# Performance work log

Measured on AMD Instinct MI355X. Metric: run time of the kernel, lower is better.

## Reference

```python
import jax, jax.numpy as jnp
import numpy as np

D_MODEL = 512
D_STATE = 128
D_CONV = 4
EXPAND = 2
NL = 10
HEADDIM = 64
D_INNER = EXPAND * D_MODEL            # 1024
NHEADS = D_INNER // HEADDIM           # 16
CONV_DIM = D_INNER + 2 * D_STATE      # 1280
D_PROJ = 2 * D_INNER + 2 * D_STATE + NHEADS  # 2320
BATCH = 8
IN_S, TOK_S = 3647, 64                # -> 57 tokens
IN_G, TOK_G = 18, 2                   # -> 9 tokens
NCLS = 55
CA_HEADS = 8
EPS = 1e-5


def setup_inputs() -> dict:
    key = jax.random.key(0)
    ks = iter(jax.random.split(key, 80))
    nrm = lambda shape, s=0.02: jax.random.normal(next(ks), shape, jnp.float32) * s
    inp = {
        "x_spectra": jax.random.normal(next(ks), (BATCH, IN_S), jnp.float32),
        "x_gaia": jax.random.normal(next(ks), (BATCH, IN_G), jnp.float32),
        "tok_w_s": nrm((TOK_S, D_MODEL), 0.05), "tok_b_s": jnp.zeros((D_MODEL,)),
        "tok_w_g": nrm((TOK_G, D_MODEL), 0.05), "tok_b_g": jnp.zeros((D_MODEL,)),
    }
    for p in ("ms", "mg"):  # spectra / gaia Mamba2 stacks, params stacked over layers
        inp[p + "_Win"] = nrm((NL, D_MODEL, D_PROJ))
        inp[p + "_conv_w"] = nrm((NL, CONV_DIM, D_CONV), 0.1)
        inp[p + "_conv_b"] = jnp.zeros((NL, CONV_DIM))
        inp[p + "_dt_bias"] = nrm((NL, NHEADS), 0.5)
        inp[p + "_A_log"] = jnp.log(jnp.tile(jnp.arange(1, NHEADS + 1, dtype=jnp.float32), (NL, 1)))
        inp[p + "_D"] = jnp.ones((NL, NHEADS))
        inp[p + "_norm_w"] = jnp.ones((NL, D_INNER))
        inp[p + "_Wout"] = nrm((NL, D_INNER, D_MODEL))
    for p in ("ca_s", "ca_g"):  # cross-attention blocks
        inp[p + "_ln_w"] = jnp.ones((D_MODEL,)); inp[p + "_ln_b"] = jnp.zeros((D_MODEL,))
        inp[p + "_in_w"] = nrm((3 * D_MODEL, D_MODEL)); inp[p + "_in_b"] = jnp.zeros((3 * D_MODEL,))
        inp[p + "_out_w"] = nrm((D_MODEL, D_MODEL)); inp[p + "_out_b"] = jnp.zeros((D_MODEL,))
    inp["cls_ln_w"] = jnp.ones((2 * D_MODEL,)); inp["cls_ln_b"] = jnp.zeros((2 * D_MODEL,))
    inp["cls_w"] = nrm((NCLS, 2 * D_MODEL)); inp["cls_b"] = jnp.zeros((NCLS,))
    return inp


def _ln(x, w, b):
    m = x.mean(-1, keepdims=True)
    v = jnp.var(x, -1, keepdims=True)
    return (x - m) * jax.lax.rsqrt(v + EPS) * w + b


def _tokenize(x, in_dim, tok_dim, w, b):
    bsz = x.shape[0]
    ntok = -(-in_dim // tok_dim)
    x = jnp.pad(x, ((0, 0), (0, ntok * tok_dim - in_dim)))
    return x.reshape(bsz, ntok, tok_dim) @ w + b  # [B, ntok, d_model]


def _mamba2_layer(x, Win, conv_w, conv_b, dt_bias, A_log, Dp, norm_w, Wout):
    bsz, L, _ = x.shape
    zxbcdt = x @ Win  # [B,L,D_PROJ]
    z, xBC, dt = jnp.split(zxbcdt, [D_INNER, D_INNER + CONV_DIM], axis=-1)
    # causal depthwise conv over time (kernel D_CONV), then SiLU
    xp = jnp.pad(xBC, ((0, 0), (D_CONV - 1, 0), (0, 0)))
    xBC = sum(conv_w[:, k] * xp[:, k:k + L, :] for k in range(D_CONV)) + conv_b
    xBC = jax.nn.silu(xBC)
    xh, Bm, Cm = jnp.split(xBC, [D_INNER, D_INNER + D_STATE], axis=-1)
    dt = jax.nn.softplus(dt + dt_bias)                 # [B,L,H]
    A = -jnp.exp(A_log)                                # [H]
    xh = xh.reshape(bsz, L, NHEADS, HEADDIM)
    dA = jnp.exp(dt * A)                               # [B,L,H] in (0,1)
    dBx = jnp.einsum('blh,bln,blhp->blhpn', dt, Bm, xh)
    # h_t = dA_t * h_{t-1} + dBx_t  via parallel associative scan over time
    def comb(e1, e2):
        a1, b1 = e1
        a2, b2 = e2
        return a1 * a2, a2[..., None, None] * b1 + b2
    _, h = jax.lax.associative_scan(comb, (dA, dBx), axis=1)  # h: [B,L,H,P,N]
    y = jnp.einsum('blhpn,bln->blhp', h, Cm) + Dp[None, None, :, None] * xh
    y = y.reshape(bsz, L, D_INNER)
    # gated RMSNorm (norm_before_gate=False): rmsnorm(y * silu(z)) * w
    y = y * jax.nn.silu(z)
    y = y * jax.lax.rsqrt(jnp.mean(y * y, -1, keepdims=True) + EPS) * norm_w
    return y @ Wout


def _mamba_stack(x, Win, cw, cb, dtb, Alog, Dp, nw, Wout):
    for i in range(NL):
        x = _mamba2_layer(x, Win[i], cw[i], cb[i], dtb[i], Alog[i], Dp[i], nw[i], Wout[i])
    return x


def _mha(q, kv, in_w, in_b, out_w, out_b):
    E = D_MODEL
    hd = E // CA_HEADS
    wq, wk, wv = in_w[:E], in_w[E:2 * E], in_w[2 * E:]
    bq, bk, bv = in_b[:E], in_b[E:2 * E], in_b[2 * E:]
    qh = (q @ wq.T + bq).reshape(*q.shape[:2], CA_HEADS, hd)
    kh = (kv @ wk.T + bk).reshape(*kv.shape[:2], CA_HEADS, hd)
    vh = (kv @ wv.T + bv).reshape(*kv.shape[:2], CA_HEADS, hd)
    scores = jnp.einsum('bqhd,bkhd->bhqk', qh, kh) / np.sqrt(hd).astype(np.float32)
    attn = jax.nn.softmax(scores, axis=-1)
    out = jnp.einsum('bhqk,bkhd->bqhd', attn, vh).reshape(*q.shape[:2], E)
    return out @ out_w.T + out_b


def reference(x_spectra, x_gaia, tok_w_s, tok_b_s, tok_w_g, tok_b_g,
              ms_Win, ms_conv_w, ms_conv_b, ms_dt_bias, ms_A_log, ms_D, ms_norm_w, ms_Wout,
              mg_Win, mg_conv_w, mg_conv_b, mg_dt_bias, mg_A_log, mg_D, mg_norm_w, mg_Wout,
              ca_s_ln_w, ca_s_ln_b, ca_s_in_w, ca_s_in_b, ca_s_out_w, ca_s_out_b,
              ca_g_ln_w, ca_g_ln_b, ca_g_in_w, ca_g_in_b, ca_g_out_w, ca_g_out_b,
              cls_ln_w, cls_ln_b, cls_w, cls_b):
    xs = _tokenize(x_spectra, IN_S, TOK_S, tok_w_s, tok_b_s)   # [B,57,512]
    xg = _tokenize(x_gaia, IN_G, TOK_G, tok_w_g, tok_b_g)      # [B,9,512]
    xs = _mamba_stack(xs, ms_Win, ms_conv_w, ms_conv_b, ms_dt_bias, ms_A_log, ms_D, ms_norm_w, ms_Wout)
    xg = _mamba_stack(xg, mg_Win, mg_conv_w, mg_conv_b, mg_dt_bias, mg_A_log, mg_D, mg_norm_w, mg_Wout)
    # cross attention (note: gaia attends to the UPDATED spectra, as in the torch code)
    xs = xs + _mha(_ln(xs, ca_s_ln_w, ca_s_ln_b), xg, ca_s_in_w, ca_s_in_b, ca_s_out_w, ca_s_out_b)
    xg = xg + _mha(_ln(xg, ca_g_ln_w, ca_g_ln_b), xs, ca_g_in_w, ca_g_in_b, ca_g_out_w, ca_g_out_b)
    fused = jnp.concatenate([xs.mean(1), xg.mean(1)], axis=-1)  # [B,1024]
    return _ln(fused, cls_ln_w, cls_ln_b) @ cls_w.T + cls_b      # [B,55]
```

## Files before the change

kernel.cpp:

```cpp
#include <hip/hip_runtime.h>
#include <cmath>

constexpr int BB    = 8;
constexpr int LS    = 57;
constexpr int LG    = 9;
constexpr int RS    = BB*LS;
constexpr int RG    = BB*LG;
constexpr int DM    = 512;
constexpr int DPROJ = 2320;
constexpr int DIN   = 1024;
constexpr int NH    = 16;
constexpr int HD    = 64;
constexpr int NLAY  = 10;

constexpr int SP_IN  = 2;
constexpr int SP_OUT = 8;
constexpr int SP_ATT = 4;

constexpr int NT_IN  = 37;
constexpr int NT_OUT = 8;
constexpr int NT_ATT = 8;
constexpr size_t WIN_PLANE  = (size_t)16*NT_IN*2048;
constexpr size_t WOUT_PLANE = (size_t)32*NT_OUT*2048;
constexpr size_t ATT_PLANE  = (size_t)16*NT_ATT*2048;

__device__ __forceinline__ float siluf(float x){ return x / (1.f + expf(-x)); }

typedef short  short8  __attribute__((ext_vector_type(8)));
typedef short  short4_ __attribute__((ext_vector_type(4)));
typedef float  f32x4   __attribute__((ext_vector_type(4)));

__device__ __forceinline__ unsigned short f2bh(float f){
    unsigned int u = __float_as_uint(f);
    u = u + 0x7FFFu + ((u >> 16) & 1u);
    return (unsigned short)(u >> 16);
}
__device__ __forceinline__ float bh2f(unsigned short h){
    return __uint_as_float(((unsigned int)h) << 16);
}

__global__ __launch_bounds__(512) void tokenize2(
    const float* __restrict__ xS, const float* __restrict__ wS, const float* __restrict__ bS,
    float* __restrict__ oS, unsigned short* __restrict__ oSh, unsigned short* __restrict__ oSl,
    const float* __restrict__ xG, const float* __restrict__ wG, const float* __restrict__ bG,
    float* __restrict__ oG, unsigned short* __restrict__ oGh, unsigned short* __restrict__ oGl)
{
    const int st = blockIdx.z;
    const int tkt = blockIdx.x, b = blockIdx.y, d = threadIdx.x;
    const int ntok = st ? LG : LS;
    if (tkt >= ntok) return;
    const float* x = st ? xG : xS;
    const float* w = st ? wG : wS;
    const float* bias = st ? bG : bS;
    float* out = st ? oG : oS;
    unsigned short* oh = st ? oGh : oSh;
    unsigned short* ol = st ? oGl : oSl;
    const int in_dim = st ? 18 : 3647, tok_dim = st ? 2 : 64;

    __shared__ float xv[64];
    if (d < tok_dim) {
        int idx = tkt*tok_dim + d;
        xv[d] = (idx < in_dim) ? x[(size_t)b*in_dim + idx] : 0.f;
    }
    __syncthreads();
    float acc = bias[d];
    for (int k=0;k<tok_dim;k++) acc += xv[k]*w[(size_t)k*DM + d];
    const size_t o = (size_t)(b*ntok + tkt)*DM + d;
    out[o] = acc;
    const unsigned short h = f2bh(acc);
    oh[o] = h;
    ol[o] = f2bh(acc - bh2f(h));
}

__global__ __launch_bounds__(256) void convert_weights(
    const float* __restrict__ winS, const float* __restrict__ winG,
    const float* __restrict__ woutS, const float* __restrict__ woutG,
    const float* __restrict__ cai, const float* __restrict__ cao,
    const float* __restrict__ cgi, const float* __restrict__ cgo,
    unsigned short* __restrict__ winh, unsigned short* __restrict__ winl,
    unsigned short* __restrict__ wouth, unsigned short* __restrict__ woutl,
    unsigned short* __restrict__ atth, unsigned short* __restrict__ attl)
{
    const int tid = threadIdx.x;
    const int bid = blockIdx.x;

    if (bid >= 8480){
        int e = bid - 8480;
        const int job = e >> 7, rem = e & 127;
        const int kt2 = rem >> 3, nt2 = rem & 7;
        const float* src =
            (job==3) ? cao : (job==7) ? cgo :
            (job< 3) ? cai + (size_t)job*512*512 : cgi + (size_t)(job-4)*512*512;
        const size_t tile = (size_t)job*ATT_PLANE + ((size_t)kt2*NT_ATT + nt2)*2048;
        const int n = tid >> 2, k8 = (tid & 3)*8;
        const float* sp = src + (size_t)(nt2*64 + n)*512 + kt2*32 + k8;
        const float4 v0 = *(const float4*)sp;
        const float4 v1 = *(const float4*)(sp+4);
        const float f[8] = {v0.x,v0.y,v0.z,v0.w,v1.x,v1.y,v1.z,v1.w};
        short8 h8, l8;
        #pragma unroll
        for (int q=0;q<8;q++){
            const unsigned short h = f2bh(f[q]);
            h8[q] = (short)h;
            l8[q] = (short)f2bh(f[q] - bh2f(h));
        }
        *(short8*)(atth + tile + tid*8) = h8;
        *(short8*)(attl + tile + tid*8) = l8;
        return;
    }

    const float* src; unsigned short *dh, *dl; int K, N, NT, nt, ktp;
    if (bid < 5920){
        const int plane = bid / 296, rem = bid % 296;
        const int s = plane & 1, layer = plane >> 1;
        src = (s ? winG : winS) + (size_t)layer*DM*DPROJ;
        dh = winh + (size_t)plane*WIN_PLANE;
        dl = winl + (size_t)plane*WIN_PLANE;
        K = DM; N = DPROJ; NT = NT_IN;
        nt = rem % 37; ktp = rem / 37;
    } else {
        const int i = bid - 5920;
        const int plane = i / 128, rem = i % 128;
        const int s = plane & 1, layer = plane >> 1;
        src = (s ? woutG : woutS) + (size_t)layer*DIN*DM;
        dh = wouth + (size_t)plane*WOUT_PLANE;
        dl = woutl + (size_t)plane*WOUT_PLANE;
        K = DIN; N = DM; NT = NT_OUT;
        nt = rem % 8; ktp = rem / 8;
    }

    __shared__ float tile[64][66];
    #pragma unroll
    for (int i=0;i<4;i++){
        const int kk = (tid>>4) + i*16;
        const int c4 = (tid&15)*4;
        const int n = nt*64 + c4;
        float4 v = {0.f,0.f,0.f,0.f};
        const float* sp = src + (size_t)(ktp*64+kk)*N + n;
        if (n + 3 < N) v = *(const float4*)sp;
        else {
            if (n   < N) v.x = sp[0];
            if (n+1 < N) v.y = sp[1];
            if (n+2 < N) v.z = sp[2];
            if (n+3 < N) v.w = sp[3];
        }
        tile[kk][c4]=v.x; tile[kk][c4+1]=v.y; tile[kk][c4+2]=v.z; tile[kk][c4+3]=v.w;
    }
    __syncthreads();

    const int n_l = tid >> 2, k8 = (tid & 3)*8;
    #pragma unroll
    for (int i=0;i<2;i++){
        const int kt2 = ktp*2 + i;
        short8 h8, l8;
        #pragma unroll
        for (int q=0;q<8;q++){
            const float f = tile[i*32 + k8 + q][n_l];
            const unsigned short h = f2bh(f);
            h8[q] = (short)h;
            l8[q] = (short)f2bh(f - bh2f(h));
        }
        const size_t off = ((size_t)kt2*NT + nt)*2048 + tid*8;
        *(short8*)(dh + off) = h8;
        *(short8*)(dl + off) = l8;
    }
}

struct GemmJob {
    const unsigned short* Ah; const unsigned short* Al;
    const unsigned short* Wh; const unsigned short* Wl;
    float* part; int M;
};

template<int NSPLIT>
__global__ __launch_bounds__(256) void gemm_mfma(GemmJob j0, GemmJob j1, GemmJob j2,
                                                 int N, int K, int NT)
{
    const int z = blockIdx.z;
    const int job = z / NSPLIT, split = z % NSPLIT;
    GemmJob jb = (job==0) ? j0 : (job==1 ? j1 : j2);
    const int bm = blockIdx.y*64, bn64 = blockIdx.x;
    const int M = jb.M;
    if (bm >= M) return;

    constexpr int SR = 40;
    __shared__ unsigned short AhS[2][64*SR], AlS[2][64*SR];
    __shared__ unsigned short BhS[2][64*SR], BlS[2][64*SR];

    const int tid = threadIdx.x;
    const int r0 = tid >> 2, k0off = (tid & 3)*8;
    const bool aok = (bm + r0 < M);
    const unsigned short* Aph = jb.Ah + (size_t)(bm+r0)*K;
    const unsigned short* Apl = jb.Al + (size_t)(bm+r0)*K;

    const int Kper = K / NSPLIT;
    const int koff = split * Kper;
    const int nk = Kper / 32;

    const size_t wbase = ((size_t)(koff >> 5)*NT + bn64)*2048 + (size_t)tid*8;
    const size_t wstep = (size_t)NT*2048;

    const short8 z8 = {0,0,0,0,0,0,0,0};
    short8 ra_h = z8, ra_l = z8, rw_h = z8, rw_l = z8;

    auto loadT = [&](int k0, int tstep){
        if (aok){
            ra_h = *(const short8*)(Aph + k0 + k0off);
            ra_l = *(const short8*)(Apl + k0 + k0off);
        } else { ra_h = z8; ra_l = z8; }
        rw_h = *(const short8*)(jb.Wh + wbase + (size_t)tstep*wstep);
        rw_l = *(const short8*)(jb.Wl + wbase + (size_t)tstep*wstep);
    };
    auto storeT = [&](int buf){
        *(short8*)&AhS[buf][r0*SR + k0off] = ra_h;
        *(short8*)&AlS[buf][r0*SR + k0off] = ra_l;
        *(short8*)&BhS[buf][r0*SR + k0off] = rw_h;
        *(short8*)&BlS[buf][r0*SR + k0off] = rw_l;
    };

    const int l = tid & 63, w = tid >> 6;
    const int fr = l & 15, kg = (l >> 4)*8;

    f32x4 acc0 = {0.f,0.f,0.f,0.f};
    f32x4 acc1 = {0.f,0.f,0.f,0.f};
    f32x4 acc2 = {0.f,0.f,0.f,0.f};
    f32x4 acc3 = {0.f,0.f,0.f,0.f};

    loadT(koff, 0);
    storeT(0);
    __syncthreads();
    for (int t=0; t<nk; ++t){
        const int cur = t & 1;
        if (t+1 < nk) loadT(koff + (t+1)*32, t+1);

        const short8 ah = *(const short8*)&AhS[cur][(w*16+fr)*SR + kg];
        const short8 al = *(const short8*)&AlS[cur][(w*16+fr)*SR + kg];
        {
            const short8 bh = *(const short8*)&BhS[cur][(fr)*SR + kg];
            const short8 bl = *(const short8*)&BlS[cur][(fr)*SR + kg];
            acc0 = __builtin_amdgcn_mfma_f32_16x16x32_bf16(ah, bh, acc0, 0,0,0);
            acc0 = __builtin_amdgcn_mfma_f32_16x16x32_bf16(ah, bl, acc0, 0,0,0);
            acc0 = __builtin_amdgcn_mfma_f32_16x16x32_bf16(al, bh, acc0, 0,0,0);
        }
        {
            const short8 bh = *(const short8*)&BhS[cur][(16+fr)*SR + kg];
            const short8 bl = *(const short8*)&BlS[cur][(16+fr)*SR + kg];
            acc1 = __builtin_amdgcn_mfma_f32_16x16x32_bf16(ah, bh, acc1, 0,0,0);
            acc1 = __builtin_amdgcn_mfma_f32_16x16x32_bf16(ah, bl, acc1, 0,0,0);
            acc1 = __builtin_amdgcn_mfma_f32_16x16x32_bf16(al, bh, acc1, 0,0,0);
        }
        {
            const short8 bh = *(const short8*)&BhS[cur][(32+fr)*SR + kg];
            const short8 bl = *(const short8*)&BlS[cur][(32+fr)*SR + kg];
            acc2 = __builtin_amdgcn_mfma_f32_16x16x32_bf16(ah, bh, acc2, 0,0,0);
            acc2 = __builtin_amdgcn_mfma_f32_16x16x32_bf16(ah, bl, acc2, 0,0,0);
            acc2 = __builtin_amdgcn_mfma_f32_16x16x32_bf16(al, bh, acc2, 0,0,0);
        }
        {
            const short8 bh = *(const short8*)&BhS[cur][(48+fr)*SR + kg];
            const short8 bl = *(const short8*)&BlS[cur][(48+fr)*SR + kg];
            acc3 = __builtin_amdgcn_mfma_f32_16x16x32_bf16(ah, bh, acc3, 0,0,0);
            acc3 = __builtin_amdgcn_mfma_f32_16x16x32_bf16(ah, bl, acc3, 0,0,0);
            acc3 = __builtin_amdgcn_mfma_f32_16x16x32_bf16(al, bh, acc3, 0,0,0);
        }
        if (t+1 < nk) storeT(cur^1);
        __syncthreads();
    }

    float* __restrict__ P = jb.part + (size_t)split*M*N;
    const int rbase = bm + w*16 + (l>>4)*4;
    const int bn = bn64*64;
    #pragma unroll
    for (int nt=0; nt<4; ++nt){
        const f32x4 a = (nt==0)?acc0 : (nt==1)?acc1 : (nt==2)?acc2 : acc3;
        const int n = bn + nt*16 + fr;
        if (n < N){
            #pragma unroll
            for (int j=0;j<4;j++){
                const int m = rbase + j;
                if (m < M) P[(size_t)m*N + n] = a[j];
            }
        }
    }
}

struct RJob { const float* part; const float* bias; const float* res; float* C;
              unsigned short* ph; unsigned short* pl; int M; };

template<int NS>
__global__ __launch_bounds__(256) void reduce_k(RJob j0, RJob j1, int N)
{
    RJob j = blockIdx.y ? j1 : j0;
    const size_t total = (size_t)j.M*N;
    const size_t i4 = ((size_t)blockIdx.x*256 + threadIdx.x)*4;
    if (i4 >= total) return;
    float4 s = *(const float4*)(j.part + i4);
    #pragma unroll
    for (int t=1;t<NS;t++){
        const float4 v = *(const float4*)(j.part + (size_t)t*total + i4);
        s.x+=v.x; s.y+=v.y; s.z+=v.z; s.w+=v.w;
    }
    const int n = (int)(i4 % (size_t)N);
    if (j.bias){ s.x+=j.bias[n]; s.y+=j.bias[n+1]; s.z+=j.bias[n+2]; s.w+=j.bias[n+3]; }
    if (j.res){ const float4 r = *(const float4*)(j.res + i4); s.x+=r.x; s.y+=r.y; s.z+=r.z; s.w+=r.w; }
    if (j.C) *(float4*)(j.C + i4) = s;
    if (j.ph){
        const float f[4] = {s.x, s.y, s.z, s.w};
        short4_ h4, l4;
        #pragma unroll
        for (int q=0;q<4;q++){
            const unsigned short h = f2bh(f[q]);
            h4[q] = (short)h;
            l4[q] = (short)f2bh(f[q] - bh2f(h));
        }
        *(short4_*)(j.ph + i4) = h4;
        *(short4_*)(j.pl + i4) = l4;
    }
}

struct PrepJob {
    const float* part;
    float* xh; float* Bc; float* Cc; float* dtw;
    const float* cw; const float* cb; const float* dtb;
    int R, L;
};

__device__ __forceinline__ float4 psum2(const float* p, size_t pstr){
    float4 a = *(const float4*)p;
    const float4 b = *(const float4*)(p + pstr);
    a.x += b.x; a.y += b.y; a.z += b.z; a.w += b.w;
    return a;
}

__global__ __launch_bounds__(256) void mamba_prep(PrepJob js, PrepJob jg)
{
    PrepJob j = blockIdx.y ? jg : js;
    const int R = j.R, L = j.L;
    constexpr int QPR = 324;
    const int q = blockIdx.x*256 + threadIdx.x;
    if (q >= R*QPR) return;
    const int r = q / QPR, qi = q % QPR;
    const int l = r % L;
    const size_t pstr = (size_t)R*DPROJ;
    const float* base = j.part + (size_t)r*DPROJ;

    if (qi < 320) {
        const int cc = qi*4;
        float tk[4][4];
        #pragma unroll
        for (int k=0;k<4;k++){
            const int lr = l - 3 + k;
            if (lr >= 0){
                float4 v = psum2(j.part + (size_t)(r-3+k)*DPROJ + 1024 + cc, pstr);
                tk[k][0]=v.x; tk[k][1]=v.y; tk[k][2]=v.z; tk[k][3]=v.w;
            } else {
                tk[k][0]=0.f; tk[k][1]=0.f; tk[k][2]=0.f; tk[k][3]=0.f;
            }
        }
        const float4 cb4 = *(const float4*)(j.cb + cc);
        const float cba[4] = {cb4.x, cb4.y, cb4.z, cb4.w};
        float out[4];
        #pragma unroll
        for (int jj=0;jj<4;jj++){
            const float4 wv = *(const float4*)(j.cw + (size_t)(cc+jj)*4);
            float v = cba[jj] + wv.x*tk[0][jj] + wv.y*tk[1][jj]
                              + wv.z*tk[2][jj] + wv.w*tk[3][jj];
            out[jj] = siluf(v);
        }
        float4 o4; o4.x=out[0]; o4.y=out[1]; o4.z=out[2]; o4.w=out[3];
        if (cc < 1024)       *(float4*)(j.xh + (size_t)r*1024 + cc)        = o4;
        else if (cc < 1152)  *(float4*)(j.Bc + (size_t)r*128 + (cc-1024))  = o4;
        else                 *(float4*)(j.Cc + (size_t)r*128 + (cc-1152))  = o4;
    } else {
        const int hd = (qi-320)*4;
        float4 s = psum2(base + 2304 + hd, pstr);
        const float4 b4 = *(const float4*)(j.dtb + hd);
        float raw[4] = {s.x+b4.x, s.y+b4.y, s.z+b4.z, s.w+b4.w};
        float4 o4;
        float* op = &o4.x;
        #pragma unroll
        for (int jj=0;jj<4;jj++)
            op[jj] = (raw[jj] > 20.f) ? raw[jj] : log1pf(expf(raw[jj]));
        *(float4*)(j.dtw + (size_t)r*16 + hd) = o4;
    }
}

__global__ __launch_bounds__(256) void mamba_cbt(
    const float* __restrict__ Bc_s, const float* __restrict__ Cc_s, float* __restrict__ cbt_s,
    const float* __restrict__ Bc_g, const float* __restrict__ Cc_g, float* __restrict__ cbt_g)
{
    const int b = blockIdx.x, st = blockIdx.y;
    const float* Bc = st ? Bc_g : Bc_s;
    const float* Cc = st ? Cc_g : Cc_s;
    float* cbt = st ? cbt_g : cbt_s;
    const int L = st ? LG : LS;
    constexpr int SB = 132;
    __shared__ float Bm[64*SB], Cm[64*SB];
    const int t = threadIdx.x;
    for (int idx = t; idx < L*32; idx += 256){
        const int l = idx >> 5, c4 = (idx & 31)*4;
        *(float4*)&Bm[l*SB + c4] = *(const float4*)(Bc + (size_t)(b*L+l)*128 + c4);
        *(float4*)&Cm[l*SB + c4] = *(const float4*)(Cc + (size_t)(b*L+l)*128 + c4);
    }
    __syncthreads();
    const int ti = t >> 4, tj = t & 15;
    float acc[4][4] = {};
    for (int k0=0;k0<128;k0+=4){
        float4 cr[4], br[4];
        #pragma unroll
        for (int a=0;a<4;a++) cr[a] = *(const float4*)&Cm[(ti+16*a)*SB + k0];
        #pragma unroll
        for (int qq=0;qq<4;qq++) br[qq] = *(const float4*)&Bm[(tj+16*qq)*SB + k0];
        #pragma unroll
        for (int a=0;a<4;a++)
            #pragma unroll
            for (int qq=0;qq<4;qq++)
                acc[a][qq] += cr[a].x*br[qq].x + cr[a].y*br[qq].y
                            + cr[a].z*br[qq].z + cr[a].w*br[qq].w;
    }
    #pragma unroll
    for (int a=0;a<4;a++){
        const int i = ti + 16*a;
        if (i < L){
            #pragma unroll
            for (int qq=0;qq<4;qq++){
                const int jj = tj + 16*qq;
                if (jj < L) cbt[(size_t)b*3840 + i*60 + jj] = acc[a][qq];
            }
        }
    }
}

__global__ __launch_bounds__(256) void mamba_y(
    const float* __restrict__ cbt_s, const float* __restrict__ xh_s, const float* __restrict__ dtw_s,
    const float* __restrict__ al_s, const float* __restrict__ Dw_s, float* __restrict__ y_s,
    const float* __restrict__ cbt_g, const float* __restrict__ xh_g, const float* __restrict__ dtw_g,
    const float* __restrict__ al_g, const float* __restrict__ Dw_g, float* __restrict__ y_g)
{
    const int h = blockIdx.x, b = blockIdx.y, st = blockIdx.z;
    const float* cbt = st ? cbt_g : cbt_s;
    const float* xh  = st ? xh_g  : xh_s;
    const float* dtw = st ? dtw_g : dtw_s;
    const float* al  = st ? al_g  : al_s;
    const float* Dw  = st ? Dw_g  : Dw_s;
    float* y = st ? y_g : y_s;
    const int L = st ? LG : LS;

    const int t = threadIdx.x;
    constexpr int SG = 60, SX = 68;
    __shared__ float Gm[64*SG], Xm[64*SX];
    __shared__ float dts[64], sps[64];

    const float Ah = -expf(al[h]);
    const float Dh = Dw[h];

    if (t < 64){
        float dtv = (t < L) ? dtw[(size_t)(b*L+t)*16 + h] : 0.f;
        float s = dtv;
        #pragma unroll
        for (int d=1; d<64; d<<=1){
            float o = __shfl_up(s, d, 64);
            if (t >= d) s += o;
        }
        dts[t] = dtv; sps[t] = s;
    }
    for (int idx = t; idx < L*16; idx += 256){
        const int l = idx >> 4, c4 = (idx & 15)*4;
        *(float4*)&Xm[l*SX + c4] = *(const float4*)(xh + (size_t)(b*L+l)*1024 + h*64 + c4);
    }
    __syncthreads();

    for (int idx = t; idx < L*15; idx += 256){
        const int i = idx/15, j4 = (idx%15)*4;
        const float4 v = *(const float4*)(cbt + (size_t)b*3840 + i*60 + j4);
        const float va[4] = {v.x, v.y, v.z, v.w};
        float g[4];
        const float si = sps[i];
        #pragma unroll
        for (int jj=0;jj<4;jj++){
            const int jc = j4 + jj;
            float gg = 0.f;
            if (jc <= i && jc < L)
                gg = expf(Ah*(si - sps[jc])) * dts[jc] * va[jj];
            g[jj] = gg;
        }
        float4 g4; g4.x=g[0]; g4.y=g[1]; g4.z=g[2]; g4.w=g[3];
        *(float4*)&Gm[i*SG + j4] = g4;
    }
    __syncthreads();

    const int ti = t >> 4, tj = t & 15;
    int la[4];
    #pragma unroll
    for (int a=0;a<4;a++) la[a] = ti + 16*a;
    float accY[4][4] = {};
    for (int m=0; m<L; ++m){
        float xr[4], gr[4];
        #pragma unroll
        for (int qq=0;qq<4;qq++) xr[qq] = Xm[m*SX + tj + 16*qq];
        #pragma unroll
        for (int a=0;a<4;a++) gr[a] = (la[a] < L) ? Gm[la[a]*SG + m] : 0.f;
        #pragma unroll
        for (int a=0;a<4;a++)
            #pragma unroll
            for (int qq=0;qq<4;qq++) accY[a][qq] = fmaf(gr[a], xr[qq], accY[a][qq]);
    }
    #pragma unroll
    for (int a=0;a<4;a++){
        if (la[a] < L){
            float* yrow = y + (size_t)(b*L + la[a])*DIN + h*HD;
            #pragma unroll
            for (int qq=0;qq<4;qq++){
                const int col = tj + 16*qq;
                yrow[col] = accY[a][qq] + Dh * Xm[la[a]*SX + col];
            }
        }
    }
}

__global__ __launch_bounds__(256) void gated_rmsnorm(
    const float* __restrict__ y_s, const float* __restrict__ part_s, const float* __restrict__ nw_s,
    unsigned short* __restrict__ oh_s, unsigned short* __restrict__ ol_s,
    const float* __restrict__ y_g, const float* __restrict__ part_g, const float* __restrict__ nw_g,
    unsigned short* __restrict__ oh_g, unsigned short* __restrict__ ol_g)
{
    int r = blockIdx.x, t = threadIdx.x;
    int st = (r >= RS);
    int row = st ? r - RS : r;
    const float* y  = (st ? y_g  : y_s) + (size_t)row*DIN;
    const float* zp = (st ? part_g : part_s) + (size_t)row*DPROJ;
    const size_t pstr = (size_t)(st ? RG : RS)*DPROJ;
    const float* nw = st ? nw_g : nw_s;
    unsigned short* oh = (st ? oh_g : oh_s) + (size_t)row*DIN;
    unsigned short* ol = (st ? ol_g : ol_s) + (size_t)row*DIN;

    float g[4]; float s2 = 0.f;
    #pragma unroll
    for (int i=0;i<4;i++){
        int idx = t + i*256;
        const float zv = zp[idx] + zp[pstr + idx];
        float gv = y[idx] * siluf(zv);
        g[i] = gv; s2 += gv*gv;
    }
    #pragma unroll
    for (int o2=32;o2;o2>>=1) s2 += __shfl_xor(s2, o2, 64);
    __shared__ float red[4];
    if ((t & 63) == 0) red[t>>6] = s2;
    __syncthreads();
    float S2 = red[0]+red[1]+red[2]+red[3];
    float scale = rsqrtf(S2*(1.f/DIN) + 1e-5f);
    #pragma unroll
    for (int i=0;i<4;i++){
        int idx = t + i*256;
        const float val = g[i]*scale*nw[idx];
        const unsigned short h = f2bh(val);
        oh[idx] = h;
        ol[idx] = f2bh(val - bh2f(h));
    }
}

__global__ __launch_bounds__(256) void ln_rows(
    const float* __restrict__ x, const float* __restrict__ w, const float* __restrict__ b,
    unsigned short* __restrict__ outh, unsigned short* __restrict__ outl, int D)
{
    int r = blockIdx.x, t = threadIdx.x;
    const float* xr = x + (size_t)r*D;
    float s = 0.f, s2 = 0.f;
    for (int i=t;i<D;i+=256){ float v = xr[i]; s += v; s2 += v*v; }
    #pragma unroll
    for (int o=32;o;o>>=1){ s += __shfl_xor(s,o,64); s2 += __shfl_xor(s2,o,64); }
    __shared__ float red[8];
    if ((t & 63) == 0){ red[t>>6] = s; red[4+(t>>6)] = s2; }
    __syncthreads();
    float S  = red[0]+red[1]+red[2]+red[3];
    float S2 = red[4]+red[5]+red[6]+red[7];
    float mean = S/D;
    float var  = S2/D - mean*mean;
    float inv  = rsqrtf(var + 1e-5f);
    for (int i=t;i<D;i+=256){
        const float val = (xr[i]-mean)*inv*w[i] + b[i];
        const unsigned short h = f2bh(val);
        outh[(size_t)r*D + i] = h;
        outl[(size_t)r*D + i] = f2bh(val - bh2f(h));
    }
}

template<int LQ, int LKV, int NS>
__global__ __launch_bounds__(256) void mha_attn2(
    const float* __restrict__ pq, const float* __restrict__ pk, const float* __restrict__ pv,
    const float* __restrict__ qb, const float* __restrict__ kb, const float* __restrict__ vb,
    int Mq, int Mkv,
    unsigned short* __restrict__ outh, unsigned short* __restrict__ outl)
{
    const int hh = blockIdx.x, b = blockIdx.y, t = threadIdx.x;
    const size_t strQ = (size_t)Mq*DM, strKV = (size_t)Mkv*DM;
    constexpr int SD = 68;
    constexpr int SS = 60;
    constexpr int QT = (LQ +15)/16;
    constexpr int KT = (LKV+15)/16;
    __shared__ float Qs[LQ*SD];
    __shared__ float Ks[LKV*SD];
    __shared__ float Vs[LKV*SD];
    __shared__ float Ps[LQ*SS];

    for (int idx = t; idx < LQ*16; idx += 256){
        const int r = idx>>4, c4 = (idx&15)*4;
        float4 v = *(const float4*)(qb + hh*64 + c4);
        const size_t off = (size_t)(b*LQ+r)*DM + hh*64 + c4;
        #pragma unroll
        for (int s=0;s<NS;s++){
            const float4 u = *(const float4*)(pq + s*strQ + off);
            v.x+=u.x; v.y+=u.y; v.z+=u.z; v.w+=u.w;
        }
        *(float4*)&Qs[r*SD+c4] = v;
    }
    for (int idx = t; idx < LKV*16; idx += 256){
        const int r = idx>>4, c4 = (idx&15)*4;
        float4 kv = *(const float4*)(kb + hh*64 + c4);
        float4 vv = *(const float4*)(vb + hh*64 + c4);
        const size_t off = (size_t)(b*LKV+r)*DM + hh*64 + c4;
        #pragma unroll
        for (int s=0;s<NS;s++){
            const float4 ku = *(const float4*)(pk + s*strKV + off);
            const float4 vu = *(const float4*)(pv + s*strKV + off);
            kv.x+=ku.x; kv.y+=ku.y; kv.z+=ku.z; kv.w+=ku.w;
            vv.x+=vu.x; vv.y+=vu.y; vv.z+=vu.z; vv.w+=vu.w;
        }
        *(float4*)&Ks[r*SD+c4] = kv;
        *(float4*)&Vs[r*SD+c4] = vv;
    }
    __syncthreads();

    const int ti = t>>4, tj = t&15;

    {
        float acc[QT][KT];
        #pragma unroll
        for (int a=0;a<QT;a++)
            #pragma unroll
            for (int q=0;q<KT;q++) acc[a][q] = 0.f;
        for (int k0=0;k0<64;k0+=4){
            float4 qr[QT], kr[KT];
            #pragma unroll
            for (int a=0;a<QT;a++){
                int rr = ti+16*a; if (rr >= LQ) rr = LQ-1;
                qr[a] = *(const float4*)&Qs[rr*SD+k0];
            }
            #pragma unroll
            for (int q=0;q<KT;q++){
                int rr = tj+16*q; if (rr >= LKV) rr = LKV-1;
                kr[q] = *(const float4*)&Ks[rr*SD+k0];
            }
            #pragma unroll
            for (int a=0;a<QT;a++)
                #pragma unroll
                for (int q=0;q<KT;q++)
                    acc[a][q] += qr[a].x*kr[q].x + qr[a].y*kr[q].y
                               + qr[a].z*kr[q].z + qr[a].w*kr[q].w;
        }
        #pragma unroll
        for (int a=0;a<QT;a++){
            const int i = ti+16*a;
            if (i < LQ){
                #pragma unroll
                for (int q=0;q<KT;q++){
                    const int jj = tj+16*q;
                    if (jj < LKV) Ps[i*SS+jj] = acc[a][q]*0.125f;
                }
            }
        }
    }
    __syncthreads();

    if (t < LQ){
        float mx = -1e30f;
        for (int j=0;j<LKV;j++) mx = fmaxf(mx, Ps[t*SS+j]);
        float se = 0.f;
        for (int j=0;j<LKV;j++){ float e = expf(Ps[t*SS+j]-mx); Ps[t*SS+j] = e; se += e; }
        const float inv = 1.f/se;
        for (int j=0;j<LKV;j++) Ps[t*SS+j] *= inv;
    }
    __syncthreads();

    {
        float o[QT][4];
        #pragma unroll
        for (int a=0;a<QT;a++){ o[a][0]=0.f; o[a][1]=0.f; o[a][2]=0.f; o[a][3]=0.f; }
        for (int m=0;m<LKV;m++){
            const float4 vv = *(const float4*)&Vs[m*SD + tj*4];
            #pragma unroll
            for (int a=0;a<QT;a++){
                const int rr = ti+16*a;
                const float pv2 = (rr < LQ) ? Ps[rr*SS+m] : 0.f;
                o[a][0] = fmaf(pv2, vv.x, o[a][0]);
                o[a][1] = fmaf(pv2, vv.y, o[a][1]);
                o[a][2] = fmaf(pv2, vv.z, o[a][2]);
                o[a][3] = fmaf(pv2, vv.w, o[a][3]);
            }
        }
        #pragma unroll
        for (int a=0;a<QT;a++){
            const int rr = ti+16*a;
            if (rr < LQ){
                short4_ h4, l4;
                #pragma unroll
                for (int q=0;q<4;q++){
                    const unsigned short h = f2bh(o[a][q]);
                    h4[q] = (short)h;
                    l4[q] = (short)f2bh(o[a][q] - bh2f(h));
                }
                const size_t off = (size_t)(b*LQ+rr)*DM + hh*64 + tj*4;
                *(short4_*)(outh + off) = h4;
                *(short4_*)(outl + off) = l4;
            }
        }
    }
}

__global__ __launch_bounds__(512) void head_fused(
    const float* __restrict__ xs, const float* __restrict__ xg,
    const float* __restrict__ lw, const float* __restrict__ lb,
    const float* __restrict__ cw, const float* __restrict__ cb,
    float* __restrict__ out)
{
    const int b = blockIdx.x, t = threadIdx.x;
    __shared__ float fr[1024];
    __shared__ float red[16];
    __shared__ float pr[55*8];
    {
        float s = 0.f;
        for (int l=0;l<LS;l++) s += xs[(size_t)(b*LS+l)*DM + t];
        fr[t] = s*(1.f/LS);
        float g = 0.f;
        for (int l=0;l<LG;l++) g += xg[(size_t)(b*LG+l)*DM + t];
        fr[512+t] = g*(1.f/LG);
    }
    __syncthreads();
    float v0 = fr[t], v1 = fr[512+t];
    float sm = v0+v1, sq = v0*v0 + v1*v1;
    #pragma unroll
    for (int o=32;o;o>>=1){ sm += __shfl_xor(sm,o,64); sq += __shfl_xor(sq,o,64); }
    if ((t&63)==0){ red[t>>6] = sm; red[8+(t>>6)] = sq; }
    __syncthreads();
    float S=0.f, Q=0.f;
    #pragma unroll
    for (int i=0;i<8;i++){ S += red[i]; Q += red[8+i]; }
    const float mean = S*(1.f/1024.f);
    const float var  = Q*(1.f/1024.f) - mean*mean;
    const float inv  = rsqrtf(var + 1e-5f);
    fr[t]     = (v0-mean)*inv*lw[t]     + lb[t];
    fr[512+t] = (v1-mean)*inv*lw[512+t] + lb[512+t];
    __syncthreads();
    {
        const int c = t & 63, pp = t >> 6;
        if (c < 55){
            float a = 0.f;
            const float* wr = cw + (size_t)c*1024 + pp*128;
            const float* xr = fr + pp*128;
            #pragma unroll 4
            for (int k=0;k<128;k++) a = fmaf(xr[k], wr[k], a);
            pr[c*8+pp] = a;
        }
    }
    __syncthreads();
    if (t < 55){
        float a = cb[t];
        #pragma unroll
        for (int p2=0;p2<8;p2++) a += pr[t*8+p2];
        out[b*55 + t] = a;
    }
}

extern "C" void kernel_launch(void* const* d_in, const int* in_sizes, int n_in,
                              void* d_out, int out_size, void* d_ws, size_t ws_size,
                              hipStream_t stream)
{
    (void)in_sizes; (void)n_in; (void)out_size; (void)ws_size;
    const float* x_spectra = (const float*)d_in[0];
    const float* x_gaia    = (const float*)d_in[1];
    const float* tok_w_s   = (const float*)d_in[2];
    const float* tok_b_s   = (const float*)d_in[3];
    const float* tok_w_g   = (const float*)d_in[4];
    const float* tok_b_g   = (const float*)d_in[5];
    const float* ms_Win    = (const float*)d_in[6];
    const float* ms_conv_w = (const float*)d_in[7];
    const float* ms_conv_b = (const float*)d_in[8];
    const float* ms_dtb    = (const float*)d_in[9];
    const float* ms_Alog   = (const float*)d_in[10];
    const float* ms_D      = (const float*)d_in[11];
    const float* ms_nw     = (const float*)d_in[12];
    const float* ms_Wout   = (const float*)d_in[13];
    const float* mg_Win    = (const float*)d_in[14];
    const float* mg_conv_w = (const float*)d_in[15];
    const float* mg_conv_b = (const float*)d_in[16];
    const float* mg_dtb    = (const float*)d_in[17];
    const float* mg_Alog   = (const float*)d_in[18];
    const float* mg_D      = (const float*)d_in[19];
    const float* mg_nw     = (const float*)d_in[20];
    const float* mg_Wout   = (const float*)d_in[21];
    const float* cas_ln_w  = (const float*)d_in[22];
    const float* cas_ln_b  = (const float*)d_in[23];
    const float* cas_in_w  = (const float*)d_in[24];
    const float* cas_in_b  = (const float*)d_in[25];
    const float* cas_out_w = (const float*)d_in[26];
    const float* cas_out_b = (const float*)d_in[27];
    const float* cag_ln_w  = (const float*)d_in[28];
    const float* cag_ln_b  = (const float*)d_in[29];
    const float* cag_in_w  = (const float*)d_in[30];
    const float* cag_in_b  = (const float*)d_in[31];
    const float* cag_out_w = (const float*)d_in[32];
    const float* cag_out_b = (const float*)d_in[33];
    const float* cls_ln_w  = (const float*)d_in[34];
    const float* cls_ln_b  = (const float*)d_in[35];
    const float* cls_w     = (const float*)d_in[36];
    const float* cls_b     = (const float*)d_in[37];

    float* p = (float*)d_ws;
    auto alloc = [&](size_t n){ float* r = p; p += n; return r; };
    float* xs       = alloc((size_t)RS*DM);
    float* xg       = alloc((size_t)RG*DM);
    float* y_s      = alloc((size_t)RS*DIN);
    float* y_g      = alloc((size_t)RG*DIN);
    float* part_inS  = alloc((size_t)SP_IN*RS*DPROJ);
    float* part_inG  = alloc((size_t)SP_IN*RG*DPROJ);
    float* part_outS = alloc((size_t)SP_OUT*RS*DM);
    float* part_outG = alloc((size_t)SP_OUT*RG*DM);
    float* part_q    = alloc((size_t)SP_ATT*RS*DM);
    float* part_k    = alloc((size_t)SP_ATT*RS*DM);
    float* part_v    = alloc((size_t)SP_ATT*RS*DM);
    float* xh_s    = alloc((size_t)RS*1024);
    float* xh_g    = alloc((size_t)RG*1024);
    float* Bc_s    = alloc((size_t)RS*128);
    float* Bc_g    = alloc((size_t)RG*128);
    float* Cc_s    = alloc((size_t)RS*128);
    float* Cc_g    = alloc((size_t)RG*128);
    float* dtw_s   = alloc((size_t)RS*16);
    float* dtw_g   = alloc((size_t)RG*16);
    float* cbt_s   = alloc((size_t)BB*3840);
    float* cbt_g   = alloc((size_t)BB*3840);

    unsigned short* up = (unsigned short*)p;
    auto ualloc = [&](size_t n){ unsigned short* r = up; up += n; return r; };
    unsigned short* xsh   = ualloc((size_t)RS*DM);
    unsigned short* xsl   = ualloc((size_t)RS*DM);
    unsigned short* xgh   = ualloc((size_t)RG*DM);
    unsigned short* xgl   = ualloc((size_t)RG*DM);
    unsigned short* ynh_s = ualloc((size_t)RS*DIN);
    unsigned short* ynl_s = ualloc((size_t)RS*DIN);
    unsigned short* ynh_g = ualloc((size_t)RG*DIN);
    unsigned short* ynl_g = ualloc((size_t)RG*DIN);
    unsigned short* lnh   = ualloc((size_t)RS*DM);
    unsigned short* lnl   = ualloc((size_t)RS*DM);
    unsigned short* aoh   = ualloc((size_t)RS*DM);
    unsigned short* aol   = ualloc((size_t)RS*DM);
    unsigned short* atth  = ualloc((size_t)8*ATT_PLANE);
    unsigned short* attl  = ualloc((size_t)8*ATT_PLANE);
    unsigned short* winh  = ualloc((size_t)20*WIN_PLANE);
    unsigned short* winl  = ualloc((size_t)20*WIN_PLANE);
    unsigned short* wouth = ualloc((size_t)20*WOUT_PLANE);
    unsigned short* woutl = ualloc((size_t)20*WOUT_PLANE);

    unsigned short* casq_h = atth + 0*ATT_PLANE; unsigned short* casq_l = attl + 0*ATT_PLANE;
    unsigned short* cask_h = atth + 1*ATT_PLANE; unsigned short* cask_l = attl + 1*ATT_PLANE;
    unsigned short* casv_h = atth + 2*ATT_PLANE; unsigned short* casv_l = attl + 2*ATT_PLANE;
    unsigned short* caso_h = atth + 3*ATT_PLANE; unsigned short* caso_l = attl + 3*ATT_PLANE;
    unsigned short* cagq_h = atth + 4*ATT_PLANE; unsigned short* cagq_l = attl + 4*ATT_PLANE;
    unsigned short* cagk_h = atth + 5*ATT_PLANE; unsigned short* cagk_l = attl + 5*ATT_PLANE;
    unsigned short* cagv_h = atth + 6*ATT_PLANE; unsigned short* cagv_l = attl + 6*ATT_PLANE;
    unsigned short* cago_h = atth + 7*ATT_PLANE; unsigned short* cago_l = attl + 7*ATT_PLANE;

    convert_weights<<<dim3(9504), 256, 0, stream>>>(
        ms_Win, mg_Win, ms_Wout, mg_Wout,
        cas_in_w, cas_out_w, cag_in_w, cag_out_w,
        winh, winl, wouth, woutl, atth, attl);

    tokenize2<<<dim3(LS, BB, 2), 512, 0, stream>>>(
        x_spectra, tok_w_s, tok_b_s, xs, xsh, xsl,
        x_gaia,    tok_w_g, tok_b_g, xg, xgh, xgl);

    const int rblkS = (RS*DM + 1023)/1024;
    const int prepBlk = (RS*324 + 255)/256;

    for (int i=0;i<NLAY;i++){
        const float* cw_s   = ms_conv_w + (size_t)i*1280*4;
        const float* cw_g   = mg_conv_w + (size_t)i*1280*4;
        const float* cbv_s  = ms_conv_b + (size_t)i*1280;
        const float* cbv_g  = mg_conv_b + (size_t)i*1280;
        const float* dtb_s  = ms_dtb  + (size_t)i*NH;
        const float* dtb_g  = mg_dtb  + (size_t)i*NH;
        const float* al_s   = ms_Alog + (size_t)i*NH;
        const float* al_g   = mg_Alog + (size_t)i*NH;
        const float* Dw_s   = ms_D    + (size_t)i*NH;
        const float* Dw_g   = mg_D    + (size_t)i*NH;
        const float* nw_s   = ms_nw   + (size_t)i*DIN;
        const float* nw_g   = mg_nw   + (size_t)i*DIN;

        const unsigned short* wih_s = winh + (size_t)(2*i+0)*WIN_PLANE;
        const unsigned short* wil_s = winl + (size_t)(2*i+0)*WIN_PLANE;
        const unsigned short* wih_g = winh + (size_t)(2*i+1)*WIN_PLANE;
        const unsigned short* wil_g = winl + (size_t)(2*i+1)*WIN_PLANE;
        const unsigned short* woh_s = wouth + (size_t)(2*i+0)*WOUT_PLANE;
        const unsigned short* wol_s = woutl + (size_t)(2*i+0)*WOUT_PLANE;
        const unsigned short* woh_g = wouth + (size_t)(2*i+1)*WOUT_PLANE;
        const unsigned short* wol_g = woutl + (size_t)(2*i+1)*WOUT_PLANE;

        GemmJob inS{xsh, xsl, wih_s, wil_s, part_inS, RS};
        GemmJob inG{xgh, xgl, wih_g, wil_g, part_inG, RG};
        gemm_mfma<SP_IN><<<dim3(NT_IN, 8, 2*SP_IN), 256, 0, stream>>>(
            inS, inG, inG, DPROJ, DM, NT_IN);

        PrepJob pjS{part_inS, xh_s, Bc_s, Cc_s, dtw_s, cw_s, cbv_s, dtb_s, RS, LS};
        PrepJob pjG{part_inG, xh_g, Bc_g, Cc_g, dtw_g, cw_g, cbv_g, dtb_g, RG, LG};
        mamba_prep<<<dim3(prepBlk, 2), 256, 0, stream>>>(pjS, pjG);

        mamba_cbt<<<dim3(BB, 2), 256, 0, stream>>>(Bc_s, Cc_s, cbt_s, Bc_g, Cc_g, cbt_g);

        mamba_y<<<dim3(NH, BB, 2), 256, 0, stream>>>(
            cbt_s, xh_s, dtw_s, al_s, Dw_s, y_s,
            cbt_g, xh_g, dtw_g, al_g, Dw_g, y_g);

        gated_rmsnorm<<<dim3(RS+RG), 256, 0, stream>>>(
            y_s, part_inS, nw_s, ynh_s, ynl_s,  y_g, part_inG, nw_g, ynh_g, ynl_g);

        GemmJob outS{ynh_s, ynl_s, woh_s, wol_s, part_outS, RS};
        GemmJob outG{ynh_g, ynl_g, woh_g, wol_g, part_outG, RG};
        gemm_mfma<SP_OUT><<<dim3(NT_OUT, 8, 2*SP_OUT), 256, 0, stream>>>(
            outS, outG, outG, DM, DIN, NT_OUT);

        RJob roS{part_outS, nullptr, nullptr, xs, xsh, xsl, RS};
        RJob roG{part_outG, nullptr, nullptr, xg, xgh, xgl, RG};
        reduce_k<SP_OUT><<<dim3(rblkS, 2), 256, 0, stream>>>(roS, roG, DM);
    }

    {
        ln_rows<<<dim3(RS), 256, 0, stream>>>(xs, cas_ln_w, cas_ln_b, lnh, lnl, DM);
        GemmJob jq{lnh, lnl, casq_h, casq_l, part_q, RS};
        GemmJob jk{xgh, xgl, cask_h, cask_l, part_k, RG};
        GemmJob jv{xgh, xgl, casv_h, casv_l, part_v, RG};
        gemm_mfma<SP_ATT><<<dim3(NT_ATT, 8, 3*SP_ATT), 256, 0, stream>>>(jq, jk, jv, DM, DM, NT_ATT);
        mha_attn2<LS,LG,SP_ATT><<<dim3(8,BB), 256, 0, stream>>>(
            part_q, part_k, part_v, cas_in_b, cas_in_b+512, cas_in_b+1024, RS, RG, aoh, aol);
        GemmJob jo{aoh, aol, caso_h, caso_l, part_outS, RS};
        gemm_mfma<SP_ATT><<<dim3(NT_ATT, 8, SP_ATT), 256, 0, stream>>>(jo, jo, jo, DM, DM, NT_ATT);
        RJob ro{part_outS, cas_out_b, xs, xs, xsh, xsl, RS};
        reduce_k<SP_ATT><<<dim3(rblkS, 1), 256, 0, stream>>>(ro, ro, DM);
    }

    {
        ln_rows<<<dim3(RG), 256, 0, stream>>>(xg, cag_ln_w, cag_ln_b, lnh, lnl, DM);
        GemmJob jq{lnh, lnl, cagq_h, cagq_l, part_q, RG};
        GemmJob jk{xsh, xsl, cagk_h, cagk_l, part_k, RS};
        GemmJob jv{xsh, xsl, cagv_h, cagv_l, part_v, RS};
        gemm_mfma<SP_ATT><<<dim3(NT_ATT, 8, 3*SP_ATT), 256, 0, stream>>>(jq, jk, jv, DM, DM, NT_ATT);
        mha_attn2<LG,LS,SP_ATT><<<dim3(8,BB), 256, 0, stream>>>(
            part_q, part_k, part_v, cag_in_b, cag_in_b+512, cag_in_b+1024, RG, RS, aoh, aol);
        GemmJob jo{aoh, aol, cago_h, cago_l, part_outS, RG};
        gemm_mfma<SP_ATT><<<dim3(NT_ATT, 2, SP_ATT), 256, 0, stream>>>(jo, jo, jo, DM, DM, NT_ATT);
        RJob ro{part_outS, cag_out_b, xg, xg, nullptr, nullptr, RG};
        reduce_k<SP_ATT><<<dim3((RG*DM+1023)/1024, 1), 256, 0, stream>>>(ro, ro, DM);
    }

    head_fused<<<dim3(BB), 512, 0, stream>>>(xs, xg, cls_ln_w, cls_ln_b, cls_w, cls_b, (float*)d_out);
}
```

Baseline: 733.0 us.

## Fuse C·Bᵀ computation into mamba_y, halve out-proj split, use nontemporal weight conversion

Removes the separate mamba_cbt kernel launch per layer by computing the C·Bᵀ product inside mamba_y directly from shared-memory B and C tiles, and folds the decay gating into that epilogue. This eliminates a launch and a global round-trip of the cbt buffer, but every head block now recomputes the same per-batch product (16x redundant work) and uses much more shared memory, which may reduce occupancy. It also halves the split-K factor for the output projection GEMM, which means fewer partial sums to reduce but less parallelism. The weight conversion kernel switches to nontemporal loads and stores.

```diff
diff --git a/kernel.cpp b/kernel.cpp
--- a/kernel.cpp
+++ b/kernel.cpp
@@ -14,7 +14,7 @@
 constexpr int NLAY  = 10;
 
 constexpr int SP_IN  = 2;
-constexpr int SP_OUT = 8;
+constexpr int SP_OUT = 4;
 constexpr int SP_ATT = 4;
 
 constexpr int NT_IN  = 37;
@@ -94,9 +94,9 @@
         const size_t tile = (size_t)job*ATT_PLANE + ((size_t)kt2*NT_ATT + nt2)*2048;
         const int n = tid >> 2, k8 = (tid & 3)*8;
         const float* sp = src + (size_t)(nt2*64 + n)*512 + kt2*32 + k8;
-        const float4 v0 = *(const float4*)sp;
-        const float4 v1 = *(const float4*)(sp+4);
-        const float f[8] = {v0.x,v0.y,v0.z,v0.w,v1.x,v1.y,v1.z,v1.w};
+        const f32x4 v0 = __builtin_nontemporal_load((const f32x4*)sp);
+        const f32x4 v1 = __builtin_nontemporal_load((const f32x4*)(sp+4));
+        const float f[8] = {v0[0],v0[1],v0[2],v0[3],v1[0],v1[1],v1[2],v1[3]};
         short8 h8, l8;
         #pragma unroll
         for (int q=0;q<8;q++){
@@ -104,8 +104,8 @@
             h8[q] = (short)h;
             l8[q] = (short)f2bh(f[q] - bh2f(h));
         }
-        *(short8*)(atth + tile + tid*8) = h8;
-        *(short8*)(attl + tile + tid*8) = l8;
+        __builtin_nontemporal_store(h8, (short8*)(atth + tile + tid*8));
+        __builtin_nontemporal_store(l8, (short8*)(attl + tile + tid*8));
         return;
     }
 
@@ -135,16 +135,16 @@
         const int kk = (tid>>4) + i*16;
         const int c4 = (tid&15)*4;
         const int n = nt*64 + c4;
-        float4 v = {0.f,0.f,0.f,0.f};
+        f32x4 v = {0.f,0.f,0.f,0.f};
         const float* sp = src + (size_t)(ktp*64+kk)*N + n;
-        if (n + 3 < N) v = *(const float4*)sp;
+        if (n + 3 < N) v = __builtin_nontemporal_load((const f32x4*)sp);
         else {
-            if (n   < N) v.x = sp[0];
-            if (n+1 < N) v.y = sp[1];
-            if (n+2 < N) v.z = sp[2];
-            if (n+3 < N) v.w = sp[3];
-        }
-        tile[kk][c4]=v.x; tile[kk][c4+1]=v.y; tile[kk][c4+2]=v.z; tile[kk][c4+3]=v.w;
+            if (n   < N) v[0] = sp[0];
+            if (n+1 < N) v[1] = sp[1];
+            if (n+2 < N) v[2] = sp[2];
+            if (n+3 < N) v[3] = sp[3];
+        }
+        tile[kk][c4]=v[0]; tile[kk][c4+1]=v[1]; tile[kk][c4+2]=v[2]; tile[kk][c4+3]=v[3];
     }
     __syncthreads();
 
@@ -161,8 +161,8 @@
             l8[q] = (short)f2bh(f - bh2f(h));
         }
         const size_t off = ((size_t)kt2*NT + nt)*2048 + tid*8;
-        *(short8*)(dh + off) = h8;
-        *(short8*)(dl + off) = l8;
+        __builtin_nontemporal_store(h8, (short8*)(dh + off));
+        __builtin_nontemporal_store(l8, (short8*)(dl + off));
     }
 }
 
@@ -385,60 +385,17 @@
     }
 }
 
-__global__ __launch_bounds__(256) void mamba_cbt(
-    const float* __restrict__ Bc_s, const float* __restrict__ Cc_s, float* __restrict__ cbt_s,
-    const float* __restrict__ Bc_g, const float* __restrict__ Cc_g, float* __restrict__ cbt_g)
-{
-    const int b = blockIdx.x, st = blockIdx.y;
-    const float* Bc = st ? Bc_g : Bc_s;
-    const float* Cc = st ? Cc_g : Cc_s;
-    float* cbt = st ? cbt_g : cbt_s;
-    const int L = st ? LG : LS;
-    constexpr int SB = 132;
-    __shared__ float Bm[64*SB], Cm[64*SB];
-    const int t = threadIdx.x;
-    for (int idx = t; idx < L*32; idx += 256){
-        const int l = idx >> 5, c4 = (idx & 31)*4;
-        *(float4*)&Bm[l*SB + c4] = *(const float4*)(Bc + (size_t)(b*L+l)*128 + c4);
-        *(float4*)&Cm[l*SB + c4] = *(const float4*)(Cc + (size_t)(b*L+l)*128 + c4);
-    }
-    __syncthreads();
-    const int ti = t >> 4, tj = t & 15;
-    float acc[4][4] = {};
-    for (int k0=0;k0<128;k0+=4){
-        float4 cr[4], br[4];
-        #pragma unroll
-        for (int a=0;a<4;a++) cr[a] = *(const float4*)&Cm[(ti+16*a)*SB + k0];
-        #pragma unroll
-        for (int qq=0;qq<4;qq++) br[qq] = *(const float4*)&Bm[(tj+16*qq)*SB + k0];
-        #pragma unroll
-        for (int a=0;a<4;a++)
-            #pragma unroll
-            for (int qq=0;qq<4;qq++)
-                acc[a][qq] += cr[a].x*br[qq].x + cr[a].y*br[qq].y
-                            + cr[a].z*br[qq].z + cr[a].w*br[qq].w;
-    }
-    #pragma unroll
-    for (int a=0;a<4;a++){
-        const int i = ti + 16*a;
-        if (i < L){
-            #pragma unroll
-            for (int qq=0;qq<4;qq++){
-                const int jj = tj + 16*qq;
-                if (jj < L) cbt[(size_t)b*3840 + i*60 + jj] = acc[a][qq];
-            }
-        }
-    }
-}
-
 __global__ __launch_bounds__(256) void mamba_y(
-    const float* __restrict__ cbt_s, const float* __restrict__ xh_s, const float* __restrict__ dtw_s,
+    const float* __restrict__ Bc_s, const float* __restrict__ Cc_s,
+    const float* __restrict__ xh_s, const float* __restrict__ dtw_s,
     const float* __restrict__ al_s, const float* __restrict__ Dw_s, float* __restrict__ y_s,
-    const float* __restrict__ cbt_g, const float* __restrict__ xh_g, const float* __restrict__ dtw_g,
+    const float* __restrict__ Bc_g, const float* __restrict__ Cc_g,
+    const float* __restrict__ xh_g, const float* __restrict__ dtw_g,
     const float* __restrict__ al_g, const float* __restrict__ Dw_g, float* __restrict__ y_g)
 {
     const int h = blockIdx.x, b = blockIdx.y, st = blockIdx.z;
-    const float* cbt = st ? cbt_g : cbt_s;
+    const float* Bc  = st ? Bc_g  : Bc_s;
+    const float* Cc  = st ? Cc_g  : Cc_s;
     const float* xh  = st ? xh_g  : xh_s;
     const float* dtw = st ? dtw_g : dtw_s;
     const float* al  = st ? al_g  : al_s;
@@ -447,7 +404,8 @@
     const int L = st ? LG : LS;
 
     const int t = threadIdx.x;
-    constexpr int SG = 60, SX = 68;
+    constexpr int SB = 132, SG = 60, SX = 68;
+    __shared__ float Bm[64*SB], Cm[64*SB];
     __shared__ float Gm[64*SG], Xm[64*SX];
     __shared__ float dts[64], sps[64];
 
@@ -464,32 +422,54 @@
         }
         dts[t] = dtv; sps[t] = s;
     }
+    for (int idx = t; idx < L*32; idx += 256){
+        const int l = idx >> 5, c4 = (idx & 31)*4;
+        *(float4*)&Bm[l*SB + c4] = *(const float4*)(Bc + (size_t)(b*L+l)*128 + c4);
+        *(float4*)&Cm[l*SB + c4] = *(const float4*)(Cc + (size_t)(b*L+l)*128 + c4);
+    }
     for (int idx = t; idx < L*16; idx += 256){
         const int l = idx >> 4, c4 = (idx & 15)*4;
         *(float4*)&Xm[l*SX + c4] = *(const float4*)(xh + (size_t)(b*L+l)*1024 + h*64 + c4);
     }
     __syncthreads();
 
-    for (int idx = t; idx < L*15; idx += 256){
-        const int i = idx/15, j4 = (idx%15)*4;
-        const float4 v = *(const float4*)(cbt + (size_t)b*3840 + i*60 + j4);
-        const float va[4] = {v.x, v.y, v.z, v.w};
-        float g[4];
-        const float si = sps[i];
-        #pragma unroll
-        for (int jj=0;jj<4;jj++){
-            const int jc = j4 + jj;
-            float gg = 0.f;
-            if (jc <= i && jc < L)
-                gg = expf(Ah*(si - sps[jc])) * dts[jc] * va[jj];
-            g[jj] = gg;
-        }
-        float4 g4; g4.x=g[0]; g4.y=g[1]; g4.z=g[2]; g4.w=g[3];
-        *(float4*)&Gm[i*SG + j4] = g4;
-    }
-    __syncthreads();
-
     const int ti = t >> 4, tj = t & 15;
+
+    {
+        float acc[4][4] = {};
+        for (int k0=0;k0<128;k0+=4){
+            float4 cr[4], br[4];
+            #pragma unroll
+            for (int a=0;a<4;a++) cr[a] = *(const float4*)&Cm[(ti+16*a)*SB + k0];
+            #pragma unroll
+            for (int qq=0;qq<4;qq++) br[qq] = *(const float4*)&Bm[(tj+16*qq)*SB + k0];
+            #pragma unroll
+            for (int a=0;a<4;a++)
+                #pragma unroll
+                for (int qq=0;qq<4;qq++)
+                    acc[a][qq] += cr[a].x*br[qq].x + cr[a].y*br[qq].y
+                                + cr[a].z*br[qq].z + cr[a].w*br[qq].w;
+        }
+        #pragma unroll
+        for (int a=0;a<4;a++){
+            const int i = ti + 16*a;
+            if (i < L){
+                const float si = sps[i];
+                #pragma unroll
+                for (int qq=0;qq<4;qq++){
+                    const int jj = tj + 16*qq;
+                    if (jj < L){
+                        float gg = 0.f;
+                        if (jj <= i)
+                            gg = expf(Ah*(si - sps[jj])) * dts[jj] * acc[a][qq];
+                        Gm[i*SG + jj] = gg;
+                    }
+                }
+            }
+        }
+    }
+    __syncthreads();
+
     int la[4];
     #pragma unroll
     for (int a=0;a<4;a++) la[a] = ti + 16*a;
@@ -836,8 +816,6 @@
     float* Cc_g    = alloc((size_t)RG*128);
     float* dtw_s   = alloc((size_t)RS*16);
     float* dtw_g   = alloc((size_t)RG*16);
-    float* cbt_s   = alloc((size_t)BB*3840);
-    float* cbt_g   = alloc((size_t)BB*3840);
 
     unsigned short* up = (unsigned short*)p;
     auto ualloc = [&](size_t n){ unsigned short* r = up; up += n; return r; };
@@ -913,11 +891,9 @@
         PrepJob pjG{part_inG, xh_g, Bc_g, Cc_g, dtw_g, cw_g, cbv_g, dtb_g, RG, LG};
         mamba_prep<<<dim3(prepBlk, 2), 256, 0, stream>>>(pjS, pjG);
 
-        mamba_cbt<<<dim3(BB, 2), 256, 0, stream>>>(Bc_s, Cc_s, cbt_s, Bc_g, Cc_g, cbt_g);
-
         mamba_y<<<dim3(NH, BB, 2), 256, 0, stream>>>(
-            cbt_s, xh_s, dtw_s, al_s, Dw_s, y_s,
-            cbt_g, xh_g, dtw_g, al_g, Dw_g, y_g);
+            Bc_s, Cc_s, xh_s, dtw_s, al_s, Dw_s, y_s,
+            Bc_g, Cc_g, xh_g, dtw_g, al_g, Dw_g, y_g);
 
         gated_rmsnorm<<<dim3(RS+RG), 256, 0, stream>>>(
             y_s, part_inS, nw_s, ynh_s, ynl_s,  y_g, part_inG, nw_g, ynh_g, ynl_g);
```

Measured after the change: 702.6 us (median of 3 runs). -4.1%, faster.
